# Performance work log

Measured on AMD Instinct MI355X. Metric: run time of the kernel, lower is better.

Reference implementation:

```python
import jax, jax.numpy as jnp
import numpy as np

B, T, C, H = 8, 1024, 768, 12
M = 8  # extra rows in feats left as zeros (n = M + B*T)
N = M + B * T


def setup_inputs() -> dict:
    key = jax.random.key(0)
    k1, k2, k3, k4, k5 = jax.random.split(key, 5)
    feats = jax.random.normal(k1, (N, C), dtype=jnp.float32)
    amask = jax.random.randint(k2, (B, T), 0, 2).astype(bool)
    Wqkv = jax.random.normal(k3, (3 * C, C), dtype=jnp.float32) * 0.02
    Wp = jax.random.normal(k4, (C, C), dtype=jnp.float32) * 0.02
    bp = jax.random.normal(k5, (C,), dtype=jnp.float32) * 0.001
    return {"feats": feats, "amask": amask, "Wqkv": Wqkv, "Wp": Wp, "bp": bp}


def reference(feats, amask, Wqkv, Wp, bp):
    b, t = amask.shape
    n, c = feats.shape
    m = n - b * t          # rows of feats not touched by attention (stay zero)
    h = H
    d = c // h
    scale = d ** -0.5
    mf = amask.reshape(-1)                      # [b*t] bool
    x = feats[m:]                               # [b*t, c]

    # MaskedLinear(qkv): gather->GEMM->scatter == dense GEMM zeroed at masked-out rows
    qkv = jnp.where(mf[:, None], x @ Wqkv.T, jnp.zeros((), x.dtype))  # [b*t, 3c]
    qkv = qkv.reshape(b, t, 3, h, d).transpose(2, 0, 3, 1, 4)          # [3,b,h,t,d]
    q, k, v = qkv[0], qkv[1], qkv[2]

    # dense SDPA (no attn mask, matching F.scaled_dot_product_attention default)
    att = jax.nn.softmax(jnp.einsum('bhqd,bhkd->bhqk', q, k) * scale, axis=-1)
    o = jnp.einsum('bhqk,bhkd->bhqd', att, v)                          # [b,h,t,d]
    o = o.transpose(0, 2, 1, 3).reshape(b * t, c)                      # [b*t, c]

    # MaskedLinear(proj) with bias; masked-out rows are zero (not bias)
    o = jnp.where(mf[:, None], o @ Wp.T + bp, jnp.zeros((), o.dtype))

    # scatter back into a zero tensor of feats' shape (first m rows zero)
    return jnp.concatenate([jnp.zeros((m, c), feats.dtype), o], axis=0)
```

## Files before the change

kernel.cpp:

```cpp
#include <hip/hip_runtime.h>
#include <hip/hip_bf16.h>


#define BB 8
#define TT 1024
#define CC 768
#define HH 12
#define DD 64
#define MM 8
#define NTOK (BB*TT)
#define NX (NTOK*CC)
#define NWQ (3*CC*CC)
#define NWP (CC*CC)
#define QSCALE 0.18033688011112042f

typedef short bf16x4 __attribute__((ext_vector_type(4)));
typedef short bf16x8 __attribute__((ext_vector_type(8)));
typedef float f32x4  __attribute__((ext_vector_type(4)));
typedef float f32x16 __attribute__((ext_vector_type(16)));
typedef unsigned int u32x2 __attribute__((ext_vector_type(2)));

__device__ __forceinline__ void gld16(const void* g, void* l) {
  __builtin_amdgcn_global_load_lds(
      (const __attribute__((address_space(1))) void*)g,
      (__attribute__((address_space(3))) void*)l, 16, 0, 0);
}

__device__ __forceinline__ short bf_rne(float f) {
  unsigned u = __float_as_uint(f);
  return (short)((u + 0x7FFFu + ((u >> 16) & 1u)) >> 16);
}
__device__ __forceinline__ short bf_split(float f, short& lo) {
  unsigned u = __float_as_uint(f);
  unsigned hb = (u + 0x7FFFu + ((u >> 16) & 1u)) >> 16;
  float r = f - __uint_as_float(hb << 16);
  lo = bf_rne(r);
  return (short)hb;
}

__global__ __launch_bounds__(256) void split_inputs(
    const float* __restrict__ x, const float* __restrict__ wq,
    const float* __restrict__ wp,
    short* __restrict__ xh, short* __restrict__ wqh,
    short* __restrict__ wph, short* __restrict__ wpl,
    float* __restrict__ out) {
  const int G0 = NX/4, G1 = G0 + NWQ/4, G2 = G1 + NWP/4;
  const int i0 = blockIdx.x * 256 + threadIdx.x;
  if (i0 < MM*CC/4) {
    float4 z = {0.f, 0.f, 0.f, 0.f};
    ((float4*)out)[i0] = z;
  }
  for (int i = i0; i < G2; i += 2048 * 256) {
    if (i < G1) {
      const float* src = (i < G0) ? x : wq;
      short* dh = (i < G0) ? xh : wqh;
      int li = (i < G0) ? i : i - G0;
      float4 v = *(const float4*)(src + (size_t)li * 4);
      short4 h;
      h.x = bf_rne(v.x); h.y = bf_rne(v.y); h.z = bf_rne(v.z); h.w = bf_rne(v.w);
      *(short4*)(dh + (size_t)li * 4) = h;
    } else {
      int li = i - G1;
      float4 v = *(const float4*)(wp + (size_t)li * 4);
      short4 h, l;
      h.x = bf_split(v.x, l.x);
      h.y = bf_split(v.y, l.y);
      h.z = bf_split(v.z, l.z);
      h.w = bf_split(v.w, l.w);
      *(short4*)(wph + (size_t)li * 4) = h;
      *(short4*)(wpl + (size_t)li * 4) = l;
    }
  }
}

template<bool TRIPLE>
__device__ __forceinline__ void gemm_core_768(
    const short* __restrict__ ah_g, const short* __restrict__ al_g,
    const short* __restrict__ bh_g, const short* __restrict__ bl_g,
    short* Ah, short* Al, short* Bh, short* Bl,
    int m0, int n0, f32x16 (&acc)[2][2],
    int& wm_o, int& wn_o) {
  const int tid = threadIdx.x;
  const int w = tid >> 6, ln = tid & 63;
  const int wm = (w >> 1) * 64, wn = (w & 1) * 64;
  const int sr = ln >> 2;
  const int sc = (((ln & 3) ^ ((ln >> 3) & 3))) * 8;
  const int l31 = ln & 31, lhi = ln >> 5;
  const int key = (l31 >> 1) & 3;
  const int c0 = 2*w, c1 = 2*w + 1;
  const short* gAh0 = ah_g + (size_t)(m0 + c0*16 + sr)*CC + sc;
  const short* gAh1 = ah_g + (size_t)(m0 + c1*16 + sr)*CC + sc;
  const short* gBh0 = bh_g + (size_t)(n0 + c0*16 + sr)*CC + sc;
  const short* gBh1 = bh_g + (size_t)(n0 + c1*16 + sr)*CC + sc;
  const short* gAl0 = TRIPLE ? al_g + (size_t)(m0 + c0*16 + sr)*CC + sc : nullptr;
  const short* gAl1 = TRIPLE ? al_g + (size_t)(m0 + c1*16 + sr)*CC + sc : nullptr;
  const short* gBl0 = TRIPLE ? bl_g + (size_t)(n0 + c0*16 + sr)*CC + sc : nullptr;
  const short* gBl1 = TRIPLE ? bl_g + (size_t)(n0 + c1*16 + sr)*CC + sc : nullptr;
  #pragma unroll
  for (int i = 0; i < 2; i++)
    #pragma unroll
    for (int j = 0; j < 2; j++)
      #pragma unroll
      for (int r = 0; r < 16; r++) acc[i][j][r] = 0.f;

  for (int it = 0; it < 24; ++it) {
    const int ko = it * 32;
    gld16(gAh0 + ko, &Ah[c0*512]);
    gld16(gAh1 + ko, &Ah[c1*512]);
    gld16(gBh0 + ko, &Bh[c0*512]);
    gld16(gBh1 + ko, &Bh[c1*512]);
    if constexpr (TRIPLE) {
      gld16(gAl0 + ko, &Al[c0*512]);
      gld16(gAl1 + ko, &Al[c1*512]);
      gld16(gBl0 + ko, &Bl[c0*512]);
      gld16(gBl1 + ko, &Bl[c1*512]);
    }
    __syncthreads();
    bf16x8 a_h[2][2], b_h[2][2];
    #pragma unroll
    for (int t = 0; t < 2; ++t)
      #pragma unroll
      for (int kc = 0; kc < 2; ++kc) {
        const int sA = ((kc*2 + lhi) ^ key) * 8;
        a_h[t][kc] = *(const bf16x8*)&Ah[(wm + t*32 + l31)*32 + sA];
        b_h[t][kc] = *(const bf16x8*)&Bh[(wn + t*32 + l31)*32 + sA];
      }
    if constexpr (TRIPLE) {
      bf16x8 a_l[2][2], b_l[2][2];
      #pragma unroll
      for (int t = 0; t < 2; ++t)
        #pragma unroll
        for (int kc = 0; kc < 2; ++kc) {
          const int sA = ((kc*2 + lhi) ^ key) * 8;
          a_l[t][kc] = *(const bf16x8*)&Al[(wm + t*32 + l31)*32 + sA];
          b_l[t][kc] = *(const bf16x8*)&Bl[(wn + t*32 + l31)*32 + sA];
        }
      #pragma unroll
      for (int mt = 0; mt < 2; ++mt)
        #pragma unroll
        for (int nt = 0; nt < 2; ++nt)
          #pragma unroll
          for (int kc = 0; kc < 2; ++kc) {
            acc[mt][nt] = __builtin_amdgcn_mfma_f32_32x32x16_bf16(
                a_h[mt][kc], b_h[nt][kc], acc[mt][nt], 0, 0, 0);
            acc[mt][nt] = __builtin_amdgcn_mfma_f32_32x32x16_bf16(
                a_h[mt][kc], b_l[nt][kc], acc[mt][nt], 0, 0, 0);
            acc[mt][nt] = __builtin_amdgcn_mfma_f32_32x32x16_bf16(
                a_l[mt][kc], b_h[nt][kc], acc[mt][nt], 0, 0, 0);
          }
    } else {
      #pragma unroll
      for (int mt = 0; mt < 2; ++mt)
        #pragma unroll
        for (int nt = 0; nt < 2; ++nt)
          #pragma unroll
          for (int kc = 0; kc < 2; ++kc)
            acc[mt][nt] = __builtin_amdgcn_mfma_f32_32x32x16_bf16(
                a_h[mt][kc], b_h[nt][kc], acc[mt][nt], 0, 0, 0);
    }
    __syncthreads();
  }
  wm_o = wm; wn_o = wn;
}

__global__ __launch_bounds__(256) void qkv_mfma(
    const short* __restrict__ xh, const short* __restrict__ wqh,
    const int* __restrict__ mask,
    short* __restrict__ qb, short* __restrict__ kb, short* __restrict__ vbt) {
  __shared__ __align__(16) short Ah[128*32], Bh[128*32];
  const int m0 = blockIdx.x * 128, n0 = blockIdx.y * 128;
  const int s = n0 / CC;
  f32x16 acc[2][2];
  int wm, wn;
  const int ln = threadIdx.x & 63;
  const int l31 = ln & 31, lhi = ln >> 5;

  if (s < 2) {
    gemm_core_768<false>(xh, nullptr, wqh, nullptr,
                         Ah, nullptr, Bh, nullptr, m0, n0, acc, wm, wn);
    short* dst = (s == 0) ? qb : kb;
    const float qs = (s == 0) ? QSCALE : 1.f;
    const int nb = n0 % CC;
    #pragma unroll
    for (int mt = 0; mt < 2; ++mt) {
      #pragma unroll
      for (int reg = 0; reg < 16; ++reg) {
        int row = m0 + wm + mt*32 + 4*lhi + (reg & 3) + 8*(reg >> 2);
        int mk = mask[row];
        int b = row >> 10, t = row & 1023;
        size_t rb = ((size_t)b * HH) * TT;
        #pragma unroll
        for (int nt = 0; nt < 2; ++nt) {
          int gnb = nb + wn + nt*32 + l31;
          int h = gnb >> 6, d = gnb & 63;
          float v = mk ? acc[mt][nt][reg] * qs : 0.f;
          dst[((rb + (size_t)h * TT) + t) * DD + d] = bf_rne(v);
        }
      }
    }
  } else {
    gemm_core_768<false>(wqh, nullptr, xh, nullptr,
                         Ah, nullptr, Bh, nullptr, n0, m0, acc, wm, wn);
    const int b = m0 >> 10, t0 = m0 & 1023;
    #pragma unroll
    for (int mt = 0; mt < 2; ++mt) {
      #pragma unroll
      for (int reg = 0; reg < 16; ++reg) {
        int f = (n0 - 2*CC) + wm + mt*32 + 4*lhi + (reg & 3) + 8*(reg >> 2);
        int h = f >> 6, d = f & 63;
        short* drow = vbt + (((size_t)(b*HH + h)*DD) + d)*TT + t0;
        #pragma unroll
        for (int nt = 0; nt < 2; ++nt) {
          int tk = wn + nt*32 + l31;
          int mk = mask[m0 + tk];
          drow[tk] = bf_rne(mk ? acc[mt][nt][reg] : 0.f);
        }
      }
    }
  }
}

__global__ __launch_bounds__(256) void proj_mfma(
    const short* __restrict__ ah_g, const short* __restrict__ al_g,
    const short* __restrict__ bh_g, const short* __restrict__ bl_g,
    const int* __restrict__ mask, const float* __restrict__ bp,
    float* __restrict__ out) {
  __shared__ __align__(16) short Ah[128*32], Al[128*32];
  __shared__ __align__(16) short Bh[128*32], Bl[128*32];
  const int m0 = blockIdx.x * 128, n0 = blockIdx.y * 128;
  f32x16 acc[2][2];
  int wm, wn;
  gemm_core_768<true>(ah_g, al_g, bh_g, bl_g, Ah, Al, Bh, Bl, m0, n0, acc, wm, wn);
  const int ln = threadIdx.x & 63;
  const int l31 = ln & 31, lhi = ln >> 5;
  #pragma unroll
  for (int mt = 0; mt < 2; ++mt) {
    #pragma unroll
    for (int reg = 0; reg < 16; ++reg) {
      int row = m0 + wm + mt*32 + 4*lhi + (reg & 3) + 8*(reg >> 2);
      int mk = mask[row];
      float* orow = out + (size_t)(MM + row) * CC;
      #pragma unroll
      for (int nt = 0; nt < 2; ++nt) {
        int gn = n0 + wn + nt*32 + l31;
        orow[gn] = mk ? acc[mt][nt][reg] + bp[gn] : 0.f;
      }
    }
  }
}

__device__ __forceinline__ bf16x4 tr64(unsigned addr, int imm) {
  bf16x4 r;
  asm volatile("ds_read_b64_tr_b16 %0, %1 offset:%c2"
               : "=v"(r) : "v"(addr), "i"(imm));
  return r;
}

__global__ __launch_bounds__(256, 3) void attn_mfma(
    const short* __restrict__ qb, const short* __restrict__ kb,
    const short* __restrict__ vbt, const int* __restrict__ mask,
    short* __restrict__ obh, short* __restrict__ obl) {
  __shared__ __align__(16) short Ks[2][64*64];
  __shared__ __align__(16) short Vt[2][64*64];
  __shared__ __align__(16) short PsT[4][2][64][16];
  const int tid = threadIdx.x, w = tid >> 6, ln = tid & 63;
  const int fl = ln & 15, fq = ln >> 4;
  const int i = blockIdx.x;
  const int bh = i % 96;
  const int q0 = (i / 96) * 128;
  const int b = bh / HH, h = bh % HH;
  const size_t baseK = (size_t)bh * TT * DD;
  const size_t baseV = (size_t)bh * DD * TT;

  bf16x8 qf[2][2];
  #pragma unroll
  for (int mt = 0; mt < 2; ++mt)
    #pragma unroll
    for (int kc = 0; kc < 2; ++kc)
      qf[mt][kc] = *(const bf16x8*)&qb[baseK +
          (size_t)(q0 + w*32 + mt*16 + fl) * DD + kc*32 + fq*8];

  f32x4 oa[2][4];
  float lsum[2][4];
  {
    f32x4 z = {0.f, 0.f, 0.f, 0.f};
    #pragma unroll
    for (int mt = 0; mt < 2; ++mt) {
      #pragma unroll
      for (int nt = 0; nt < 4; ++nt) oa[mt][nt] = z;
      #pragma unroll
      for (int r = 0; r < 4; ++r) lsum[mt][r] = 0.f;
    }
  }

  const unsigned ps_rd =
      (unsigned)(size_t)(&PsT[0][0][0][0]) + w*4096 + fq*256 + fl*8;

  const int r1 = tid >> 3, r2 = r1 + 32;
  const int g1 = ((ln & 7) ^ (r1 & 7)) * 8;
  const int g2 = ((ln & 7) ^ (r2 & 7)) * 8;
  const short* kg1 = &kb[baseK + (size_t)r1 * DD + g1];
  const short* kg2 = &kb[baseK + (size_t)r2 * DD + g2];
  const short* vg1 = &vbt[baseV + (size_t)r1 * TT + g1];
  const short* vg2 = &vbt[baseV + (size_t)r2 * TT + g2];

  auto stage = [&](int p, int kt) {
    gld16(kg1 + (size_t)kt * 64 * DD, &Ks[p][w * 512]);
    gld16(kg2 + (size_t)kt * 64 * DD, &Ks[p][2048 + w * 512]);
    gld16(vg1 + kt * 64, &Vt[p][w * 512]);
    gld16(vg2 + kt * 64, &Vt[p][2048 + w * 512]);
  };

  stage(0, 0);
  asm volatile("s_waitcnt vmcnt(0)" ::: "memory");
  __builtin_amdgcn_s_barrier();
  __builtin_amdgcn_sched_barrier(0);

  for (int kt = 0; kt < 16; ++kt) {
    const int p = kt & 1;
    if (kt < 15) stage(p ^ 1, kt + 1);

    bf16x8 kf[4][2];
    #pragma unroll
    for (int nt = 0; nt < 4; ++nt)
      #pragma unroll
      for (int kc = 0; kc < 2; ++kc) {
        const int sl = ((kc*4 + fq) ^ (fl & 7)) * 8;
        kf[nt][kc] = *(const bf16x8*)&Ks[p][(nt*16 + fl)*64 + sl];
      }

    f32x4 s[2][4];
    {
      f32x4 z = {0.f, 0.f, 0.f, 0.f};
      #pragma unroll
      for (int mt = 0; mt < 2; ++mt)
        #pragma unroll
        for (int nt = 0; nt < 4; ++nt) s[mt][nt] = z;
    }
    __builtin_amdgcn_s_setprio(1);
    #pragma unroll
    for (int mt = 0; mt < 2; ++mt)
      #pragma unroll
      for (int nt = 0; nt < 4; ++nt) {
        s[mt][nt] = __builtin_amdgcn_mfma_f32_16x16x32_bf16(
            qf[mt][0], kf[nt][0], s[mt][nt], 0, 0, 0);
        s[mt][nt] = __builtin_amdgcn_mfma_f32_16x16x32_bf16(
            qf[mt][1], kf[nt][1], s[mt][nt], 0, 0, 0);
      }
    __builtin_amdgcn_s_setprio(0);

    bf16x8 vf[4][2];
    #pragma unroll
    for (int nt = 0; nt < 4; ++nt)
      #pragma unroll
      for (int kc = 0; kc < 2; ++kc) {
        const int sl = ((kc*4 + fq) ^ (fl & 7)) * 8;
        vf[nt][kc] = *(const bf16x8*)&Vt[p][(nt*16 + fl)*64 + sl];
      }

    #pragma unroll
    for (int mt = 0; mt < 2; ++mt)
      #pragma unroll
      for (int nt = 0; nt < 4; ++nt) {
        unsigned u0 = __float_as_uint(__builtin_amdgcn_exp2f(s[mt][nt][0]));
        unsigned u1 = __float_as_uint(__builtin_amdgcn_exp2f(s[mt][nt][1]));
        unsigned u2 = __float_as_uint(__builtin_amdgcn_exp2f(s[mt][nt][2]));
        unsigned u3 = __float_as_uint(__builtin_amdgcn_exp2f(s[mt][nt][3]));
        lsum[mt][0] += __uint_as_float(u0 & 0xFFFF0000u);
        lsum[mt][1] += __uint_as_float(u1 & 0xFFFF0000u);
        lsum[mt][2] += __uint_as_float(u2 & 0xFFFF0000u);
        lsum[mt][3] += __uint_as_float(u3 & 0xFFFF0000u);
        u32x2 pw;
        pw[0] = (u0 >> 16) | (u1 & 0xFFFF0000u);
        pw[1] = (u2 >> 16) | (u3 & 0xFFFF0000u);
        *(u32x2*)&PsT[w][mt][nt*16 + fl][fq*4] = pw;
      }

    asm volatile("s_waitcnt lgkmcnt(0)" ::: "memory");

    bf16x8 pf[2][2];
    #pragma unroll
    for (int mt = 0; mt < 2; ++mt)
      #pragma unroll
      for (int kc = 0; kc < 2; ++kc) {
        bf16x4 lo = tr64(ps_rd, mt*2048 + kc*1024);
        bf16x4 hi = tr64(ps_rd, mt*2048 + kc*1024 + 128);
        pf[mt][kc] = __builtin_shufflevector(lo, hi, 0, 1, 2, 3, 4, 5, 6, 7);
      }
    asm volatile("s_waitcnt lgkmcnt(0)" ::: "memory");
    __builtin_amdgcn_sched_barrier(0);

    __builtin_amdgcn_s_setprio(1);
    #pragma unroll
    for (int mt = 0; mt < 2; ++mt)
      #pragma unroll
      for (int nt = 0; nt < 4; ++nt) {
        oa[mt][nt] = __builtin_amdgcn_mfma_f32_16x16x32_bf16(
            pf[mt][0], vf[nt][0], oa[mt][nt], 0, 0, 0);
        oa[mt][nt] = __builtin_amdgcn_mfma_f32_16x16x32_bf16(
            pf[mt][1], vf[nt][1], oa[mt][nt], 0, 0, 0);
      }
    __builtin_amdgcn_s_setprio(0);

    asm volatile("s_waitcnt vmcnt(0)" ::: "memory");
    __builtin_amdgcn_s_barrier();
    __builtin_amdgcn_sched_barrier(0);
  }

  #pragma unroll
  for (int mt = 0; mt < 2; ++mt)
    #pragma unroll
    for (int r = 0; r < 4; ++r) {
      float v = lsum[mt][r];
      v += __shfl_xor(v, 1);
      v += __shfl_xor(v, 2);
      v += __shfl_xor(v, 4);
      v += __shfl_xor(v, 8);
      lsum[mt][r] = v;
    }

  #pragma unroll
  for (int mt = 0; mt < 2; ++mt)
    #pragma unroll
    for (int r = 0; r < 4; ++r) {
      int tok = b * TT + q0 + w*32 + mt*16 + fq*4 + r;
      int mk = mask[tok];
      float inv = 1.f / lsum[mt][r];
      size_t ro = (size_t)tok * CC + h * DD;
      #pragma unroll
      for (int nt = 0; nt < 4; ++nt) {
        float v = mk ? oa[mt][nt][r] * inv : 0.f;
        short lo, hi = bf_split(v, lo);
        obh[ro + nt*16 + fl] = hi;
        obl[ro + nt*16 + fl] = lo;
      }
    }
}

extern "C" void kernel_launch(void* const* d_in, const int* in_sizes, int n_in,
                              void* d_out, int out_size, void* d_ws, size_t ws_size,
                              hipStream_t stream) {
  const float* feats = (const float*)d_in[0];
  const int*   mask  = (const int*)d_in[1];
  const float* Wqkv  = (const float*)d_in[2];
  const float* Wp    = (const float*)d_in[3];
  const float* bp    = (const float*)d_in[4];
  float* out = (float*)d_out;

  short* qb   = (short*)d_ws;
  short* kb   = qb + NX;
  short* vbt  = kb + NX;
  short* S_hi = vbt + NX;
  short* S_lo = S_hi + NX;
  short* wqh  = S_lo + NX;
  short* wph  = wqh + NWQ;
  short* wpl  = wph + NWP;

  split_inputs<<<dim3(2048), dim3(256), 0, stream>>>(
      feats + (size_t)MM * CC, Wqkv, Wp, S_hi, wqh, wph, wpl, out);
  qkv_mfma<<<dim3(NTOK/128, 3*CC/128), dim3(256), 0, stream>>>(
      S_hi, wqh, mask, qb, kb, vbt);
  attn_mfma<<<dim3(96 * (TT/128)), dim3(256), 0, stream>>>(
      qb, kb, vbt, mask, S_hi, S_lo);
  proj_mfma<<<dim3(NTOK/128, CC/128), dim3(256), 0, stream>>>(
      S_hi, S_lo, wph, wpl, mask, bp, out);
}
```

Baseline: 212.9 us.

## Double-buffer LDS tiles in GEMM core to overlap global loads with MFMA

Adds a two-stage LDS ping-pong in the shared 768-K GEMM core so the next K-slice is fetched via global_load_lds while the current slice is multiplied. Explicit vmcnt waits and barriers replace the two __syncthreads per iteration. The aim is to hide global-memory latency in both the QKV and projection GEMMs. LDS use doubles, which may lower occupancy, especially for the triple-bf16 projection kernel (64KB).

```diff
diff --git a/kernel.cpp b/kernel.cpp
--- a/kernel.cpp
+++ b/kernel.cpp
@@ -103,27 +103,30 @@
       #pragma unroll
       for (int r = 0; r < 16; r++) acc[i][j][r] = 0.f;
 
-  for (int it = 0; it < 24; ++it) {
-    const int ko = it * 32;
-    gld16(gAh0 + ko, &Ah[c0*512]);
-    gld16(gAh1 + ko, &Ah[c1*512]);
-    gld16(gBh0 + ko, &Bh[c0*512]);
-    gld16(gBh1 + ko, &Bh[c1*512]);
+  auto stage = [&](int hf, int it) {
+    const int ko = it * 32, off = hf * 4096;
+    gld16(gAh0 + ko, &Ah[off + c0*512]);
+    gld16(gAh1 + ko, &Ah[off + c1*512]);
+    gld16(gBh0 + ko, &Bh[off + c0*512]);
+    gld16(gBh1 + ko, &Bh[off + c1*512]);
     if constexpr (TRIPLE) {
-      gld16(gAl0 + ko, &Al[c0*512]);
-      gld16(gAl1 + ko, &Al[c1*512]);
-      gld16(gBl0 + ko, &Bl[c0*512]);
-      gld16(gBl1 + ko, &Bl[c1*512]);
-    }
-    __syncthreads();
+      gld16(gAl0 + ko, &Al[off + c0*512]);
+      gld16(gAl1 + ko, &Al[off + c1*512]);
+      gld16(gBl0 + ko, &Bl[off + c0*512]);
+      gld16(gBl1 + ko, &Bl[off + c1*512]);
+    }
+  };
+
+  auto compute = [&](int hf) {
+    const int off = hf * 4096;
     bf16x8 a_h[2][2], b_h[2][2];
     #pragma unroll
     for (int t = 0; t < 2; ++t)
       #pragma unroll
       for (int kc = 0; kc < 2; ++kc) {
         const int sA = ((kc*2 + lhi) ^ key) * 8;
-        a_h[t][kc] = *(const bf16x8*)&Ah[(wm + t*32 + l31)*32 + sA];
-        b_h[t][kc] = *(const bf16x8*)&Bh[(wn + t*32 + l31)*32 + sA];
+        a_h[t][kc] = *(const bf16x8*)&Ah[off + (wm + t*32 + l31)*32 + sA];
+        b_h[t][kc] = *(const bf16x8*)&Bh[off + (wn + t*32 + l31)*32 + sA];
       }
     if constexpr (TRIPLE) {
       bf16x8 a_l[2][2], b_l[2][2];
@@ -132,8 +135,8 @@
         #pragma unroll
         for (int kc = 0; kc < 2; ++kc) {
           const int sA = ((kc*2 + lhi) ^ key) * 8;
-          a_l[t][kc] = *(const bf16x8*)&Al[(wm + t*32 + l31)*32 + sA];
-          b_l[t][kc] = *(const bf16x8*)&Bl[(wn + t*32 + l31)*32 + sA];
+          a_l[t][kc] = *(const bf16x8*)&Al[off + (wm + t*32 + l31)*32 + sA];
+          b_l[t][kc] = *(const bf16x8*)&Bl[off + (wn + t*32 + l31)*32 + sA];
         }
       #pragma unroll
       for (int mt = 0; mt < 2; ++mt)
@@ -158,7 +161,27 @@
             acc[mt][nt] = __builtin_amdgcn_mfma_f32_32x32x16_bf16(
                 a_h[mt][kc], b_h[nt][kc], acc[mt][nt], 0, 0, 0);
     }
-    __syncthreads();
+  };
+
+  stage(0, 0);
+
+  #pragma unroll 1
+  for (int it = 0; it < 24; ++it) {
+    const int hf = it & 1;
+    if (it < 23) {
+      stage(hf ^ 1, it + 1);
+      if constexpr (TRIPLE)
+        asm volatile("s_waitcnt vmcnt(8)" ::: "memory");
+      else
+        asm volatile("s_waitcnt vmcnt(4)" ::: "memory");
+    } else {
+      asm volatile("s_waitcnt vmcnt(0)" ::: "memory");
+    }
+    __builtin_amdgcn_s_barrier();
+    __builtin_amdgcn_sched_barrier(0);
+    compute(hf);
+    __builtin_amdgcn_s_barrier();
+    __builtin_amdgcn_sched_barrier(0);
   }
   wm_o = wm; wn_o = wn;
 }
@@ -167,7 +190,7 @@
     const short* __restrict__ xh, const short* __restrict__ wqh,
     const int* __restrict__ mask,
     short* __restrict__ qb, short* __restrict__ kb, short* __restrict__ vbt) {
-  __shared__ __align__(16) short Ah[128*32], Bh[128*32];
+  __shared__ __align__(16) short Ah[2*128*32], Bh[2*128*32];
   const int m0 = blockIdx.x * 128, n0 = blockIdx.y * 128;
   const int s = n0 / CC;
   f32x16 acc[2][2];
@@ -225,8 +248,8 @@
     const short* __restrict__ bh_g, const short* __restrict__ bl_g,
     const int* __restrict__ mask, const float* __restrict__ bp,
     float* __restrict__ out) {
-  __shared__ __align__(16) short Ah[128*32], Al[128*32];
-  __shared__ __align__(16) short Bh[128*32], Bl[128*32];
+  __shared__ __align__(16) short Ah[2*128*32], Al[2*128*32];
+  __shared__ __align__(16) short Bh[2*128*32], Bl[2*128*32];
   const int m0 = blockIdx.x * 128, n0 = blockIdx.y * 128;
   f32x16 acc[2][2];
   int wm, wn;
```

Result: slower. 227.0 us (+6.6%).

## Use 64x128 tiles for QKV GEMM with a flattened, column-major block order

Applied to the files above, without the earlier changes.

Adds a 64x128 GEMM core for the QKV projection, with four waves each computing a 32x64 subtile, replacing the 128x128 tile. This doubles the block count to 2304 and sets launch bounds to 6 blocks per SM. Blocks are ordered so consecutive blocks share the same weight tile, which should improve L2 reuse and occupancy. In exchange each output element has less operand reuse and each block does more loads and barriers per FLOP.

```diff
diff --git a/kernel.cpp b/kernel.cpp
--- a/kernel.cpp
+++ b/kernel.cpp
@@ -163,58 +163,104 @@
   wm_o = wm; wn_o = wn;
 }
 
-__global__ __launch_bounds__(256) void qkv_mfma(
+__device__ __forceinline__ void gemm_core_64x128(
+    const short* __restrict__ a_g, const short* __restrict__ b_g,
+    short* Ah, short* Bh, int m0, int n0, f32x16 (&acc)[2],
+    int& wm_o, int& wn_o) {
+  const int tid = threadIdx.x;
+  const int w = tid >> 6, ln = tid & 63;
+  const int wm = (w >> 1) * 32, wn = (w & 1) * 64;
+  const int l31 = ln & 31, lhi = ln >> 5;
+  const int key = (l31 >> 1) & 3;
+
+  const int rA = w*16 + (ln >> 2);
+  const short* gA = a_g + (size_t)(m0 + rA)*CC
+                        + ((ln & 3) ^ ((rA >> 1) & 3)) * 8;
+  const int rB0 = w*32 + (ln >> 2), rB1 = rB0 + 16;
+  const short* gB0 = b_g + (size_t)(n0 + rB0)*CC
+                         + ((ln & 3) ^ ((rB0 >> 1) & 3)) * 8;
+  const short* gB1 = b_g + (size_t)(n0 + rB1)*CC
+                         + ((ln & 3) ^ ((rB1 >> 1) & 3)) * 8;
+
+  #pragma unroll
+  for (int j = 0; j < 2; j++)
+    #pragma unroll
+    for (int r = 0; r < 16; r++) acc[j][r] = 0.f;
+
+  for (int it = 0; it < 24; ++it) {
+    const int ko = it * 32;
+    gld16(gA  + ko, &Ah[w*512]);
+    gld16(gB0 + ko, &Bh[w*1024]);
+    gld16(gB1 + ko, &Bh[w*1024 + 512]);
+    __syncthreads();
+    bf16x8 a_h[2], b_h[2][2];
+    #pragma unroll
+    for (int kc = 0; kc < 2; ++kc) {
+      const int sA = ((kc*2 + lhi) ^ key) * 8;
+      a_h[kc]    = *(const bf16x8*)&Ah[(wm + l31)*32 + sA];
+      b_h[0][kc] = *(const bf16x8*)&Bh[(wn + l31)*32 + sA];
+      b_h[1][kc] = *(const bf16x8*)&Bh[(wn + 32 + l31)*32 + sA];
+    }
+    #pragma unroll
+    for (int nt = 0; nt < 2; ++nt)
+      #pragma unroll
+      for (int kc = 0; kc < 2; ++kc)
+        acc[nt] = __builtin_amdgcn_mfma_f32_32x32x16_bf16(
+            a_h[kc], b_h[nt][kc], acc[nt], 0, 0, 0);
+    __syncthreads();
+  }
+  wm_o = wm; wn_o = wn;
+}
+
+__global__ __launch_bounds__(256, 6) void qkv_mfma(
     const short* __restrict__ xh, const short* __restrict__ wqh,
     const int* __restrict__ mask,
     short* __restrict__ qb, short* __restrict__ kb, short* __restrict__ vbt) {
-  __shared__ __align__(16) short Ah[128*32], Bh[128*32];
-  const int m0 = blockIdx.x * 128, n0 = blockIdx.y * 128;
-  const int s = n0 / CC;
-  f32x16 acc[2][2];
+  __shared__ __align__(16) short Ah[64*32], Bh[128*32];
+  f32x16 acc[2];
   int wm, wn;
   const int ln = threadIdx.x & 63;
   const int l31 = ln & 31, lhi = ln >> 5;
-
-  if (s < 2) {
-    gemm_core_768<false>(xh, nullptr, wqh, nullptr,
-                         Ah, nullptr, Bh, nullptr, m0, n0, acc, wm, wn);
-    short* dst = (s == 0) ? qb : kb;
-    const float qs = (s == 0) ? QSCALE : 1.f;
-    const int nb = n0 % CC;
-    #pragma unroll
-    for (int mt = 0; mt < 2; ++mt) {
-      #pragma unroll
-      for (int reg = 0; reg < 16; ++reg) {
-        int row = m0 + wm + mt*32 + 4*lhi + (reg & 3) + 8*(reg >> 2);
-        int mk = mask[row];
-        int b = row >> 10, t = row & 1023;
-        size_t rb = ((size_t)b * HH) * TT;
-        #pragma unroll
-        for (int nt = 0; nt < 2; ++nt) {
-          int gnb = nb + wn + nt*32 + l31;
-          int h = gnb >> 6, d = gnb & 63;
-          float v = mk ? acc[mt][nt][reg] * qs : 0.f;
-          dst[((rb + (size_t)h * TT) + t) * DD + d] = bf_rne(v);
-        }
+  const int bid = blockIdx.x;
+
+  if (bid < 1536) {
+    const int tn = bid >> 7, tm = bid & 127;
+    const int m0 = tm * 64, n0 = tn * 128;
+    gemm_core_64x128(xh, wqh, Ah, Bh, m0, n0, acc, wm, wn);
+    short* dst = (n0 < CC) ? qb : kb;
+    const float qs = (n0 < CC) ? QSCALE : 1.f;
+    const int nb = (n0 < CC) ? n0 : n0 - CC;
+    #pragma unroll
+    for (int reg = 0; reg < 16; ++reg) {
+      int row = m0 + wm + 4*lhi + (reg & 3) + 8*(reg >> 2);
+      int mk = mask[row];
+      int b = row >> 10, t = row & 1023;
+      size_t rb = ((size_t)b * HH) * TT;
+      #pragma unroll
+      for (int nt = 0; nt < 2; ++nt) {
+        int gnb = nb + wn + nt*32 + l31;
+        int h = gnb >> 6, d = gnb & 63;
+        float v = mk ? acc[nt][reg] * qs : 0.f;
+        dst[((rb + (size_t)h * TT) + t) * DD + d] = bf_rne(v);
       }
     }
   } else {
-    gemm_core_768<false>(wqh, nullptr, xh, nullptr,
-                         Ah, nullptr, Bh, nullptr, n0, m0, acc, wm, wn);
-    const int b = m0 >> 10, t0 = m0 & 1023;
-    #pragma unroll
-    for (int mt = 0; mt < 2; ++mt) {
-      #pragma unroll
-      for (int reg = 0; reg < 16; ++reg) {
-        int f = (n0 - 2*CC) + wm + mt*32 + 4*lhi + (reg & 3) + 8*(reg >> 2);
-        int h = f >> 6, d = f & 63;
-        short* drow = vbt + (((size_t)(b*HH + h)*DD) + d)*TT + t0;
-        #pragma unroll
-        for (int nt = 0; nt < 2; ++nt) {
-          int tk = wn + nt*32 + l31;
-          int mk = mask[m0 + tk];
-          drow[tk] = bf_rne(mk ? acc[mt][nt][reg] : 0.f);
-        }
+    const int vb = bid - 1536;
+    const int wv = vb >> 6, tv = vb & 63;
+    const int m0w = 2*CC + wv*64;
+    const int t0 = tv * 128;
+    gemm_core_64x128(wqh, xh, Ah, Bh, m0w, t0, acc, wm, wn);
+    const int b = t0 >> 10, tb = t0 & 1023;
+    #pragma unroll
+    for (int reg = 0; reg < 16; ++reg) {
+      int f = wv*64 + wm + 4*lhi + (reg & 3) + 8*(reg >> 2);
+      int h = f >> 6, d = f & 63;
+      short* drow = vbt + (((size_t)(b*HH + h)*DD) + d)*TT + tb;
+      #pragma unroll
+      for (int nt = 0; nt < 2; ++nt) {
+        int tk = wn + nt*32 + l31;
+        int mk = mask[t0 + tk];
+        drow[tk] = bf_rne(mk ? acc[nt][reg] : 0.f);
       }
     }
   }
@@ -458,7 +504,7 @@
 
   split_inputs<<<dim3(2048), dim3(256), 0, stream>>>(
       feats + (size_t)MM * CC, Wqkv, Wp, S_hi, wqh, wph, wpl, out);
-  qkv_mfma<<<dim3(NTOK/128, 3*CC/128), dim3(256), 0, stream>>>(
+  qkv_mfma<<<dim3(2304), dim3(256), 0, stream>>>(
       S_hi, wqh, mask, qb, kb, vbt);
   attn_mfma<<<dim3(96 * (TT/128)), dim3(256), 0, stream>>>(
       qb, kb, vbt, mask, S_hi, S_lo);
```

After: 221.0 us. 1.04x slower.
